# Performance work log

Hardware: AMD Instinct MI355X
Metric: run time of the kernel (lower is better)

## Reference

```python
import jax, jax.numpy as jnp
import numpy as np

N = 2048      # n_nodes
Q = 1024      # n_query
S = 512       # n_seeds
NBINS = 20
NPOWS = 5
HOP = 2


def _divide_no_nan(a, b):
    safe_b = jnp.where(b == 0, 1.0, b)
    return jnp.where(b == 0, 0.0, a / safe_b)


def _local_calib(g, calib_w):
    # soft-binning calibration: broadcast against NBINS Gaussian bumps
    parts = np.linspace(0.0, 1.0, NBINS)
    tmp = parts[1:] - parts[:-1]
    sig = np.zeros_like(parts)
    sig[:-1] += tmp
    sig[1:] += tmp
    sig[1:-1] /= 2.0
    sig = sig / 50.0  # sigma_div
    bases = jnp.asarray(parts, dtype=g.dtype)
    sigmas = jnp.asarray(sig, dtype=g.dtype)
    mask = (g > 0).astype(g.dtype)
    d = g[..., None] - bases            # [N, N, NBINS]
    z = jnp.exp(-(d * d) / sigmas)
    z = _divide_no_nan(z, jnp.sum(z, axis=-1, keepdims=True))
    probs = jax.nn.softmax(calib_w)     # use_cumsum=False
    out = jnp.sum(z * probs, axis=-1)
    return out * mask


def _normalize_by_degrees(g):
    # diag(1/sqrt(rowsum)) @ g @ diag(1/sqrt(colsum)), done as scaling
    dl = jnp.sqrt(jnp.sum(g, axis=1))
    dr = jnp.sqrt(jnp.sum(g, axis=0))
    left = _divide_no_nan(jnp.ones_like(dl), dl)
    right = _divide_no_nan(jnp.ones_like(dr), dr)
    return left[:, None] * g * right[None, :]


def _global_calib(g, w, b):
    # edge standardization + learned power series + elu shift
    mask = (g > 0).astype(g.dtype)
    n_nz = jnp.sum(mask)
    mean = jnp.sum(g) / n_nz
    d = g - mean
    var = jnp.sum(mask * d * d) / n_nz
    gn = (g - mean) / jnp.sqrt(var) * mask
    mult = jnp.abs(gn)
    mult_safe = jnp.where(mult == 0, 1.0, mult)
    sqr = jnp.where(mult == 0, 0.0, gn * jnp.sqrt(mult_safe) / mult_safe)
    powers = [gn, sqr]
    last = gn
    for _ in range(NPOWS - 2):
        last = last * mult
        powers.append(last)
    stacked = jnp.stack(powers, axis=-1)           # [Q, S, NPOWS]
    out = jnp.einsum('qsp,p->qs', stacked, w[:, 0]) + b[0]
    out = jax.nn.elu(out) + 1.0
    return out * mask


def setup_inputs() -> dict:
    key = jax.random.key(0)
    k1, k2, k3, k4, k5, k6 = jax.random.split(key, 6)
    u = jax.random.uniform(k1, (N, N), dtype=jnp.float32)
    sparsity = (jax.random.uniform(k2, (N, N)) > 0.5).astype(jnp.float32)
    graph = u * sparsity
    # CalibLocalLayer default init for calib_w
    parts = np.linspace(0.0, 1.0, NBINS)
    w_init = np.log(parts + 1e-06) - np.mean(parts)
    calib_w = jnp.asarray(w_init, dtype=jnp.float32)
    global_w = jnp.ones((NPOWS, 1), dtype=jnp.float32)
    global_b = jnp.zeros((1,), dtype=jnp.float32)
    # NodeImportanceLayer init from graph column degrees
    cw = np.array(_divide_no_nan(1.0, jnp.sqrt(jnp.sum(graph, axis=0))))
    cw = np.log(cw + 1e-06)
    cw = cw - np.mean(cw)
    col_weights = jnp.asarray(cw[None, :], dtype=jnp.float32)
    query_ids = jax.random.randint(k3, (Q,), 0, N, dtype=jnp.int32)
    seed_ids = jax.random.randint(k4, (S,), 0, N, dtype=jnp.int32)
    return {
        'graph': graph, 'calib_w': calib_w, 'global_w': global_w,
        'global_b': global_b, 'col_weights': col_weights,
        'query_ids': query_ids, 'seed_ids': seed_ids,
    }


def reference(graph, calib_w, global_w, global_b, col_weights, query_ids, seed_ids):
    n = graph.shape[0]
    g = _local_calib(graph, calib_w)               # calib_before_lp = 'local'
    g = _normalize_by_degrees(g)
    cw = jax.nn.softmax(col_weights, axis=1) * n   # node importance
    g = g * cw
    graph_mult = g
    gq = g[query_ids]                              # [Q, N]
    for _ in range(HOP - 1):
        gq = gq @ graph_mult                       # multi-hop propagation
    # zero self-edge: column j == query node id
    diag_mask = (jnp.arange(n)[None, :] != query_ids[:, None]).astype(gq.dtype)
    gq = gq * diag_mask
    gq = gq[:, seed_ids]                           # [Q, S]
    gq = _global_calib(gq, global_w, global_b)     # calib_after_lp = 'global'
    out = _divide_no_nan(gq, jnp.sum(gq, axis=1, keepdims=True))
    return out
```

## Files before the change

### kernel.cpp

```cpp
#include <hip/hip_runtime.h>
#include <hip/hip_bf16.h>

#define NDIM 2048
#define QDIM 1024
#define SDIM 512
#define NBINS 20
#define GT_TK 64
#define GT_TS 64

typedef __attribute__((ext_vector_type(8))) short bf16x8;
typedef __attribute__((ext_vector_type(4))) float f32x4;

__device__ __forceinline__ unsigned short f2bf(float f) {
  unsigned int u = __builtin_bit_cast(unsigned int, f);
  u += 0x7fffu + ((u >> 16) & 1u);
  return (unsigned short)(u >> 16);
}
__device__ __forceinline__ float bf2f(unsigned short h) {
  return __builtin_bit_cast(float, (unsigned int)h << 16);
}
__device__ __forceinline__ float guard_rsqrt(float x) {
  return x > 0.f ? 1.0f / sqrtf(x) : 0.f;
}

__global__ __launch_bounds__(256) void k_calib(const float* __restrict__ graph,
                                               const float* __restrict__ calib_w,
                                               unsigned short* __restrict__ g0bf,
                                               float* __restrict__ rowsum,
                                               float* __restrict__ colsum) {
  __shared__ float sp[NBINS];
  __shared__ float lrowp[4][4];
  __shared__ float lcol[NDIM];
  int t = threadIdx.x;
  if (t == 0) {
    float m = -1e30f;
    for (int b = 0; b < NBINS; b++) m = fmaxf(m, calib_w[b]);
    float e[NBINS]; float s = 0.f;
    for (int b = 0; b < NBINS; b++) { e[b] = __expf(calib_w[b] - m); s += e[b]; }
    float inv = 1.0f / s;
    for (int b = 0; b < NBINS; b++) sp[b] = e[b] * inv;
  }
  __syncthreads();
  const float q1 = __expf(-950.0f / 361.0f);
  const float q2 = __expf(-950.0f * 4.0f / 361.0f);
  const float q3 = __expf(-950.0f * 9.0f / 361.0f);
  const float q4 = __expf(-950.0f * 16.0f / 361.0f);
  int r0 = blockIdx.x * 4;
  float colacc[8] = {0.f,0.f,0.f,0.f,0.f,0.f,0.f,0.f};
  #pragma unroll
  for (int r = 0; r < 4; r++) {
    int row = r0 + r;
    const float4* src = (const float4*)(graph + (size_t)row * NDIM);
    float4 in0 = src[t * 2];
    float4 in1 = src[t * 2 + 1];
    float gv[8] = {in0.x, in0.y, in0.z, in0.w, in1.x, in1.y, in1.z, in1.w};
    unsigned short ov[8];
    float rs = 0.f;
    #pragma unroll
    for (int i = 0; i < 8; i++) {
      float g = gv[i];
      float v = 0.f;
      if (g > 0.f) {
        int bstar = (int)floorf(g * 19.0f + 0.5f);
        int lo = bstar - 2;
        lo = lo < 0 ? 0 : (lo > NBINS - 5 ? NBINS - 5 : lo);
        float delta = g - (float)lo * (1.0f / 19.0f);
        float rr = __expf(100.0f * delta);
        float r2_ = rr * rr;
        float r3_ = r2_ * rr;
        float r4_ = r2_ * r2_;
        float den = 1.0f + q1 * rr + q2 * r2_ + q3 * r3_ + q4 * r4_;
        float num = sp[lo] + q1 * rr * sp[lo+1] + q2 * r2_ * sp[lo+2]
                  + q3 * r3_ * sp[lo+3] + q4 * r4_ * sp[lo+4];
        v = num / den;
      }
      ov[i] = f2bf(v);
      rs += v;
      colacc[i] += v;
    }
    uint4 packed;
    __builtin_memcpy(&packed, ov, 16);
    *(uint4*)(g0bf + (size_t)row * NDIM + t * 8) = packed;
    #pragma unroll
    for (int m = 32; m > 0; m >>= 1) rs += __shfl_xor(rs, m);
    if ((t & 63) == 0) lrowp[r][t >> 6] = rs;
  }
  *(float4*)&lcol[t * 8]     = *(float4*)&colacc[0];
  *(float4*)&lcol[t * 8 + 4] = *(float4*)&colacc[4];
  __syncthreads();
  if (t < 4) rowsum[r0 + t] = lrowp[t][0] + lrowp[t][1] + lrowp[t][2] + lrowp[t][3];
  #pragma unroll
  for (int j = 0; j < 8; j++)
    atomicAdd(&colsum[j * 256 + t], lcol[j * 256 + t]);
}

__global__ __launch_bounds__(512) void k_gatherBt(const unsigned short* __restrict__ g0bf,
                                                  const int* __restrict__ sid,
                                                  const float* __restrict__ rowsum,
                                                  const float* __restrict__ colsum,
                                                  const float* __restrict__ col_w,
                                                  unsigned short* __restrict__ Bt) {
  __shared__ int scol[GT_TS];
  __shared__ float lrsc[GT_TS];
  __shared__ float lmv[GT_TK];
  __shared__ unsigned short lt[GT_TS][GT_TK + 4];
  int t = threadIdx.x;
  int k0 = blockIdx.x * GT_TK;
  int s0 = blockIdx.y * GT_TS;
  if (t < GT_TS) {
    int col = sid[s0 + t];
    scol[t] = col;
    lrsc[t] = guard_rsqrt(colsum[col]) * __expf(col_w[col]);
  } else if (t < GT_TS + GT_TK) {
    int k = k0 + t - GT_TS;
    lmv[t - GT_TS] = guard_rsqrt(rowsum[k]) * guard_rsqrt(colsum[k]) * __expf(col_w[k]);
  }
  __syncthreads();
  int tx = t & 63;
  int ty = t >> 6;
  #pragma unroll
  for (int r = ty; r < GT_TK; r += 8) {
    float v = bf2f(g0bf[(size_t)(k0 + r) * NDIM + scol[tx]]);
    lt[tx][r] = f2bf(v * lmv[r] * lrsc[tx]);
  }
  __syncthreads();
  int s = t >> 3;
  int kk = (t & 7) * 8;
  uint4 val;
  __builtin_memcpy(&val, &lt[s][kk], 16);
  *(uint4*)(Bt + (size_t)(s0 + s) * NDIM + k0 + kk) = val;
}

__global__ __launch_bounds__(256) void k_mfma_stats(const unsigned short* __restrict__ g0bf,
                                                    const unsigned short* __restrict__ Bt,
                                                    const int* __restrict__ qid,
                                                    const int* __restrict__ sid,
                                                    const float* __restrict__ rowsum,
                                                    float* __restrict__ C,
                                                    double* __restrict__ stats_p) {
  __shared__ float r1[256], r2[256]; __shared__ int rc[256];
  int t = threadIdx.x;
  int lane = t & 63, wave = t >> 6;
  int bid = blockIdx.x;
  int m0 = (bid >> 3) * 64 + (wave >> 1) * 32;
  int n0 = (bid & 7) * 64 + (wave & 1) * 32;
  int fr = lane & 15;
  int kq = (lane >> 4) * 8;
  int qa0 = qid[m0 + fr];
  int qa1 = qid[m0 + 16 + fr];
  const unsigned short* Ap0 = g0bf + (size_t)qa0 * NDIM + kq;
  const unsigned short* Ap1 = g0bf + (size_t)qa1 * NDIM + kq;
  const unsigned short* Bp0 = Bt + (size_t)(n0 + fr) * NDIM + kq;
  const unsigned short* Bp1 = Bp0 + (size_t)16 * NDIM;
  f32x4 acc00 = {0.f,0.f,0.f,0.f}, acc01 = acc00, acc10 = acc00, acc11 = acc00;
  #pragma unroll 4
  for (int i = 0; i < 64; i++) {
    int off = i * 32;
    bf16x8 a0 = *(const bf16x8*)(Ap0 + off);
    bf16x8 a1 = *(const bf16x8*)(Ap1 + off);
    bf16x8 b0 = *(const bf16x8*)(Bp0 + off);
    bf16x8 b1 = *(const bf16x8*)(Bp1 + off);
    acc00 = __builtin_amdgcn_mfma_f32_16x16x32_bf16(a0, b0, acc00, 0, 0, 0);
    acc01 = __builtin_amdgcn_mfma_f32_16x16x32_bf16(a0, b1, acc01, 0, 0, 0);
    acc10 = __builtin_amdgcn_mfma_f32_16x16x32_bf16(a1, b0, acc10, 0, 0, 0);
    acc11 = __builtin_amdgcn_mfma_f32_16x16x32_bf16(a1, b1, acc11, 0, 0, 0);
  }
  int r0_ = (lane >> 4) * 4;
  int c0_ = lane & 15;
  int sc0 = sid[n0 + c0_];
  int sc1 = sid[n0 + 16 + c0_];
  float s = 0.f, s2 = 0.f; int c = 0;
  #pragma unroll
  for (int r = 0; r < 4; r++) {
    int mrow0 = m0 + r0_ + r;
    int mrow1 = mrow0 + 16;
    int qv0 = qid[mrow0];
    int qv1 = qid[mrow1];
    float lq0 = guard_rsqrt(rowsum[qv0]);
    float lq1 = guard_rsqrt(rowsum[qv1]);
    float v00 = acc00[r] * lq0; if (sc0 == qv0) v00 = 0.f;
    float v01 = acc01[r] * lq0; if (sc1 == qv0) v01 = 0.f;
    float v10 = acc10[r] * lq1; if (sc0 == qv1) v10 = 0.f;
    float v11 = acc11[r] * lq1; if (sc1 == qv1) v11 = 0.f;
    C[(size_t)mrow0 * SDIM + n0 + c0_]      = v00;
    C[(size_t)mrow0 * SDIM + n0 + 16 + c0_] = v01;
    C[(size_t)mrow1 * SDIM + n0 + c0_]      = v10;
    C[(size_t)mrow1 * SDIM + n0 + 16 + c0_] = v11;
    if (v00 > 0.f) { s += v00; s2 += v00 * v00; c++; }
    if (v01 > 0.f) { s += v01; s2 += v01 * v01; c++; }
    if (v10 > 0.f) { s += v10; s2 += v10 * v10; c++; }
    if (v11 > 0.f) { s += v11; s2 += v11 * v11; c++; }
  }
  r1[t] = s; r2[t] = s2; rc[t] = c; __syncthreads();
  for (int st = 128; st > 0; st >>= 1) {
    if (t < st) { r1[t] += r1[t+st]; r2[t] += r2[t+st]; rc[t] += rc[t+st]; }
    __syncthreads();
  }
  if (t == 0) {
    stats_p[bid * 3 + 0] = (double)r1[0];
    stats_p[bid * 3 + 1] = (double)r2[0];
    stats_p[bid * 3 + 2] = (double)rc[0];
  }
}

__global__ void k_final(const float* __restrict__ C, const double* __restrict__ stats_p,
                        const float* __restrict__ gw, const float* __restrict__ gb,
                        float* __restrict__ out) {
  __shared__ float red[256];
  int q = blockIdx.x, t = threadIdx.x;
  double ss = 0.0, ss2 = 0.0, sc = 0.0;
  for (int j = 0; j < 128; j++) {
    ss  += stats_p[j * 3 + 0];
    ss2 += stats_p[j * 3 + 1];
    sc  += stats_p[j * 3 + 2];
  }
  double mean_d = ss / sc;
  double var_d = ss2 / sc - mean_d * mean_d;
  float mean = (float)mean_d;
  float invstd = (float)(1.0 / sqrt(var_d));
  float w0 = gw[0], w1 = gw[1], w2 = gw[2], w3 = gw[3], w4 = gw[4], bb = gb[0];
  float vals[2]; float rs = 0.f;
  #pragma unroll
  for (int p = 0; p < 2; p++) {
    int s = t + p * 256;
    float x = C[(size_t)q * SDIM + s];
    float v = 0.f;
    if (x > 0.f) {
      float gn = (x - mean) * invstd;
      float m = fabsf(gn);
      float sgnsq = (m > 0.f) ? (gn / m) * sqrtf(m) : 0.f;
      float acc = w0 * gn + w1 * sgnsq;
      float gm = gn * m; acc += w2 * gm;
      gm *= m;           acc += w3 * gm;
      gm *= m;           acc += w4 * gm;
      acc += bb;
      v = (acc > 0.f ? acc : __expf(acc) - 1.f) + 1.f;
    }
    vals[p] = v; rs += v;
  }
  red[t] = rs; __syncthreads();
  for (int st = 128; st > 0; st >>= 1) { if (t < st) red[t] += red[t+st]; __syncthreads(); }
  float tot = red[0];
  float inv = tot > 0.f ? 1.0f / tot : 0.f;
  #pragma unroll
  for (int p = 0; p < 2; p++) {
    int s = t + p * 256;
    out[(size_t)q * SDIM + s] = vals[p] * inv;
  }
}

extern "C" void kernel_launch(void* const* d_in, const int* in_sizes, int n_in,
                              void* d_out, int out_size, void* d_ws, size_t ws_size,
                              hipStream_t stream) {
  const float* graph    = (const float*)d_in[0];
  const float* calib_w  = (const float*)d_in[1];
  const float* global_w = (const float*)d_in[2];
  const float* global_b = (const float*)d_in[3];
  const float* col_w    = (const float*)d_in[4];
  const int*   qid      = (const int*)d_in[5];
  const int*   sid      = (const int*)d_in[6];
  float* out = (float*)d_out;

  char* ws = (char*)d_ws;
  float*  colsum  = (float*)(ws + 0);
  float*  rowsum  = (float*)(ws + 8192);
  double* stats_p = (double*)(ws + 16384);
  unsigned short* g0bf = (unsigned short*)(ws + 65536);
  unsigned short* Bt   = (unsigned short*)(ws + 65536 + 8388608);
  float*  C      = (float*)(ws + 65536 + 8388608 + 2097152);

  k_calib<<<NDIM / 4, 256, 0, stream>>>(graph, calib_w, g0bf, rowsum, colsum);
  k_gatherBt<<<dim3(NDIM / GT_TK, SDIM / GT_TS), 512, 0, stream>>>(g0bf, sid, rowsum, colsum, col_w, Bt);
  k_mfma_stats<<<128, 256, 0, stream>>>(g0bf, Bt, qid, sid, rowsum, C, stats_p);
  k_final<<<QDIM, 256, 0, stream>>>(C, stats_p, global_w, global_b, out);
}
```

Before: 142.6 us.

## Split GEMM K across waves with LDS reduction and tree-reduce stats in final kernel

The GEMM kernel now uses 512 blocks of 32x32 output tiles instead of 128 blocks of 64x64. Each of the four waves computes a quarter of the K dimension, and the partial tiles are summed through shared memory. The aim is to fill more compute units, since 128 blocks is under the MI355X's CU count. The 512 per-block partial statistics go into separate arrays, and k_final sums them with a parallel shared-memory tree instead of every thread looping serially. The cost is an LDS round-trip and an extra barrier, plus less reuse of A and B per block.

Result: faster. 123.0 us (median of 2 runs) (-13.7%).

```diff
diff --git a/kernel.cpp b/kernel.cpp
--- a/kernel.cpp
+++ b/kernel.cpp
@@ -137,24 +137,27 @@
                                                     const int* __restrict__ sid,
                                                     const float* __restrict__ rowsum,
                                                     float* __restrict__ C,
-                                                    double* __restrict__ stats_p) {
+                                                    double* __restrict__ stats_s,
+                                                    double* __restrict__ stats_s2,
+                                                    double* __restrict__ stats_c) {
+  __shared__ float lacc[4][32 * 33];
   __shared__ float r1[256], r2[256]; __shared__ int rc[256];
   int t = threadIdx.x;
   int lane = t & 63, wave = t >> 6;
-  int bid = blockIdx.x;
-  int m0 = (bid >> 3) * 64 + (wave >> 1) * 32;
-  int n0 = (bid & 7) * 64 + (wave & 1) * 32;
+  int n0 = blockIdx.x * 32;
+  int m0 = blockIdx.y * 32;
   int fr = lane & 15;
   int kq = (lane >> 4) * 8;
+  int kbase = wave * 512;
   int qa0 = qid[m0 + fr];
   int qa1 = qid[m0 + 16 + fr];
-  const unsigned short* Ap0 = g0bf + (size_t)qa0 * NDIM + kq;
-  const unsigned short* Ap1 = g0bf + (size_t)qa1 * NDIM + kq;
-  const unsigned short* Bp0 = Bt + (size_t)(n0 + fr) * NDIM + kq;
+  const unsigned short* Ap0 = g0bf + (size_t)qa0 * NDIM + kbase + kq;
+  const unsigned short* Ap1 = g0bf + (size_t)qa1 * NDIM + kbase + kq;
+  const unsigned short* Bp0 = Bt + (size_t)(n0 + fr) * NDIM + kbase + kq;
   const unsigned short* Bp1 = Bp0 + (size_t)16 * NDIM;
   f32x4 acc00 = {0.f,0.f,0.f,0.f}, acc01 = acc00, acc10 = acc00, acc11 = acc00;
   #pragma unroll 4
-  for (int i = 0; i < 64; i++) {
+  for (int i = 0; i < 16; i++) {
     int off = i * 32;
     bf16x8 a0 = *(const bf16x8*)(Ap0 + off);
     bf16x8 a1 = *(const bf16x8*)(Ap1 + off);
@@ -167,29 +170,27 @@
   }
   int r0_ = (lane >> 4) * 4;
   int c0_ = lane & 15;
-  int sc0 = sid[n0 + c0_];
-  int sc1 = sid[n0 + 16 + c0_];
+  float* L = lacc[wave];
+  #pragma unroll
+  for (int r = 0; r < 4; r++) {
+    L[(r0_ + r) * 33 + c0_]            = acc00[r];
+    L[(r0_ + r) * 33 + 16 + c0_]       = acc01[r];
+    L[(16 + r0_ + r) * 33 + c0_]       = acc10[r];
+    L[(16 + r0_ + r) * 33 + 16 + c0_]  = acc11[r];
+  }
+  __syncthreads();
   float s = 0.f, s2 = 0.f; int c = 0;
   #pragma unroll
-  for (int r = 0; r < 4; r++) {
-    int mrow0 = m0 + r0_ + r;
-    int mrow1 = mrow0 + 16;
-    int qv0 = qid[mrow0];
-    int qv1 = qid[mrow1];
-    float lq0 = guard_rsqrt(rowsum[qv0]);
-    float lq1 = guard_rsqrt(rowsum[qv1]);
-    float v00 = acc00[r] * lq0; if (sc0 == qv0) v00 = 0.f;
-    float v01 = acc01[r] * lq0; if (sc1 == qv0) v01 = 0.f;
-    float v10 = acc10[r] * lq1; if (sc0 == qv1) v10 = 0.f;
-    float v11 = acc11[r] * lq1; if (sc1 == qv1) v11 = 0.f;
-    C[(size_t)mrow0 * SDIM + n0 + c0_]      = v00;
-    C[(size_t)mrow0 * SDIM + n0 + 16 + c0_] = v01;
-    C[(size_t)mrow1 * SDIM + n0 + c0_]      = v10;
-    C[(size_t)mrow1 * SDIM + n0 + 16 + c0_] = v11;
-    if (v00 > 0.f) { s += v00; s2 += v00 * v00; c++; }
-    if (v01 > 0.f) { s += v01; s2 += v01 * v01; c++; }
-    if (v10 > 0.f) { s += v10; s2 += v10 * v10; c++; }
-    if (v11 > 0.f) { s += v11; s2 += v11 * v11; c++; }
+  for (int e = t; e < 1024; e += 256) {
+    int row = e >> 5, col = e & 31;
+    int li = row * 33 + col;
+    float v = lacc[0][li] + lacc[1][li] + lacc[2][li] + lacc[3][li];
+    int mrow = m0 + row;
+    int qv = qid[mrow];
+    v *= guard_rsqrt(rowsum[qv]);
+    if (sid[n0 + col] == qv) v = 0.f;
+    C[(size_t)mrow * SDIM + n0 + col] = v;
+    if (v > 0.f) { s += v; s2 += v * v; c++; }
   }
   r1[t] = s; r2[t] = s2; rc[t] = c; __syncthreads();
   for (int st = 128; st > 0; st >>= 1) {
@@ -197,25 +198,32 @@
     __syncthreads();
   }
   if (t == 0) {
-    stats_p[bid * 3 + 0] = (double)r1[0];
-    stats_p[bid * 3 + 1] = (double)r2[0];
-    stats_p[bid * 3 + 2] = (double)rc[0];
-  }
-}
-
-__global__ void k_final(const float* __restrict__ C, const double* __restrict__ stats_p,
+    int sidx = blockIdx.y * 16 + blockIdx.x;
+    stats_s[sidx]  = (double)r1[0];
+    stats_s2[sidx] = (double)r2[0];
+    stats_c[sidx]  = (double)rc[0];
+  }
+}
+
+__global__ void k_final(const float* __restrict__ C,
+                        const double* __restrict__ stats_s,
+                        const double* __restrict__ stats_s2,
+                        const double* __restrict__ stats_c,
                         const float* __restrict__ gw, const float* __restrict__ gb,
                         float* __restrict__ out) {
+  __shared__ double d1[256], d2[256], d3[256];
   __shared__ float red[256];
   int q = blockIdx.x, t = threadIdx.x;
-  double ss = 0.0, ss2 = 0.0, sc = 0.0;
-  for (int j = 0; j < 128; j++) {
-    ss  += stats_p[j * 3 + 0];
-    ss2 += stats_p[j * 3 + 1];
-    sc  += stats_p[j * 3 + 2];
-  }
-  double mean_d = ss / sc;
-  double var_d = ss2 / sc - mean_d * mean_d;
+  d1[t] = stats_s[t]  + stats_s[t + 256];
+  d2[t] = stats_s2[t] + stats_s2[t + 256];
+  d3[t] = stats_c[t]  + stats_c[t + 256];
+  __syncthreads();
+  for (int st = 128; st > 0; st >>= 1) {
+    if (t < st) { d1[t] += d1[t+st]; d2[t] += d2[t+st]; d3[t] += d3[t+st]; }
+    __syncthreads();
+  }
+  double mean_d = d1[0] / d3[0];
+  double var_d = d2[0] / d3[0] - mean_d * mean_d;
   float mean = (float)mean_d;
   float invstd = (float)(1.0 / sqrt(var_d));
   float w0 = gw[0], w1 = gw[1], w2 = gw[2], w3 = gw[3], w4 = gw[4], bb = gb[0];
@@ -262,15 +270,17 @@
   float* out = (float*)d_out;
 
   char* ws = (char*)d_ws;
-  float*  colsum  = (float*)(ws + 0);
-  float*  rowsum  = (float*)(ws + 8192);
-  double* stats_p = (double*)(ws + 16384);
+  float*  colsum   = (float*)(ws + 0);
+  float*  rowsum   = (float*)(ws + 8192);
+  double* stats_s  = (double*)(ws + 16384);
+  double* stats_s2 = (double*)(ws + 20480);
+  double* stats_c  = (double*)(ws + 24576);
   unsigned short* g0bf = (unsigned short*)(ws + 65536);
   unsigned short* Bt   = (unsigned short*)(ws + 65536 + 8388608);
   float*  C      = (float*)(ws + 65536 + 8388608 + 2097152);
 
   k_calib<<<NDIM / 4, 256, 0, stream>>>(graph, calib_w, g0bf, rowsum, colsum);
   k_gatherBt<<<dim3(NDIM / GT_TK, SDIM / GT_TS), 512, 0, stream>>>(g0bf, sid, rowsum, colsum, col_w, Bt);
-  k_mfma_stats<<<128, 256, 0, stream>>>(g0bf, Bt, qid, sid, rowsum, C, stats_p);
-  k_final<<<QDIM, 256, 0, stream>>>(C, stats_p, global_w, global_b, out);
-}
+  k_mfma_stats<<<dim3(SDIM / 32, QDIM / 32), 256, 0, stream>>>(g0bf, Bt, qid, sid, rowsum, C, stats_s, stats_s2, stats_c);
+  k_final<<<QDIM, 256, 0, stream>>>(C, stats_s, stats_s2, stats_c, global_w, global_b, out);
+}
```
